# Optimization experiments

Measured on AMD Instinct MI355X. Metric: run time of the kernel, lower is better.

## Reference

```python
import jax, jax.numpy as jnp
import numpy as np

N_NODES = 50000
N_EDGES = 800000
EDGE_F = 96
NODE_F = 256
GLOB_F = 64
HIDDEN = 1024
N_GRAPHS = 8
MLP_IN = NODE_F + 3 * EDGE_F + GLOB_F  # 608


def setup_inputs() -> dict:
    key = jax.random.key(0)
    ks = jax.random.split(key, 9)
    x = jax.random.normal(ks[0], (N_NODES, NODE_F), dtype=jnp.float32)
    edge_attr = jax.random.normal(ks[1], (N_EDGES, EDGE_F), dtype=jnp.float32)
    u = jax.random.normal(ks[2], (N_GRAPHS, GLOB_F), dtype=jnp.float32)
    W1 = jax.random.normal(ks[3], (MLP_IN, HIDDEN), dtype=jnp.float32) * (1.0 / np.sqrt(MLP_IN))
    b1 = jax.random.normal(ks[4], (HIDDEN,), dtype=jnp.float32) * 0.01
    W2 = jax.random.normal(ks[5], (HIDDEN, NODE_F), dtype=jnp.float32) * (1.0 / np.sqrt(HIDDEN))
    b2 = jax.random.normal(ks[6], (NODE_F,), dtype=jnp.float32) * 0.01
    edge_index = jax.random.randint(ks[7], (2, N_EDGES), 0, N_NODES, dtype=jnp.int64 if jax.config.jax_enable_x64 else jnp.int32)
    batch = jnp.sort(jax.random.randint(ks[8], (N_NODES,), 0, N_GRAPHS, dtype=jnp.int32))
    return {"x": x, "edge_attr": edge_attr, "u": u, "W1": W1, "b1": b1,
            "W2": W2, "b2": b2, "edge_index": edge_index, "batch": batch}


def reference(x, edge_attr, u, W1, b1, W2, b2, edge_index, batch):
    col = edge_index[1]  # destination node for each edge
    n = x.shape[0]
    # sum / max / mean segment reductions over edges -> per-node features
    out1 = jax.ops.segment_sum(edge_attr, col, num_segments=n)                     # [N, E_F]
    cnt = jax.ops.segment_sum(jnp.ones((edge_attr.shape[0], 1), edge_attr.dtype), col, num_segments=n)  # [N,1]
    out2 = jax.ops.segment_max(edge_attr, col, num_segments=n)
    out2 = jnp.where(cnt > 0, out2, jnp.zeros_like(out2))  # torch_scatter gives 0 for empty segments
    out3 = out1 / jnp.maximum(cnt, 1.0)                    # mean; 0 for empty segments
    h = jnp.concatenate([x, out1, out2, out3, u[batch]], axis=1)  # [N, 608]
    h = jax.nn.relu(h @ W1 + b1) @ W2 + b2                        # node MLP
    return h + x  # residual
```

## Files before the change

kernel.cpp:

```cpp
#include <hip/hip_runtime.h>
#include <stdint.h>

#define N_NODES 50000
#define N_EDGES 800000
#define EDGE_F  96
#define NODE_F  256
#define GLOB_F  64
#define HIDDEN  1024
#define MLP_IN  608
#define KP      640
#define M_PAD   50176
#define SCAN_BLOCKS 196
#define NT1     10

typedef __bf16 bf16;
typedef __bf16 bf16x8 __attribute__((ext_vector_type(8)));
typedef float  f32x4  __attribute__((ext_vector_type(4)));

typedef __attribute__((address_space(1))) unsigned int gu32;
typedef __attribute__((address_space(3))) unsigned int lu32;

__device__ __forceinline__ void glds16(const void* g, void* l) {
    __builtin_amdgcn_global_load_lds((const gu32*)g, (lu32*)l, 16, 0, 0);
}

static constexpr size_t H_OFF    = 0;
static constexpr size_t H_BYTES  = (size_t)M_PAD * KP * 2;
static constexpr size_t HID_OFF  = H_OFF + H_BYTES;
static constexpr size_t HID_BYTES= (size_t)M_PAD * HIDDEN * 2;
static constexpr size_t W1T_OFF  = HID_OFF + HID_BYTES;
static constexpr size_t W1T_BYTES= (size_t)HIDDEN * KP * 2;
static constexpr size_t W2T_OFF  = W1T_OFF + W1T_BYTES;
static constexpr size_t W2T_BYTES= (size_t)NODE_F * HIDDEN * 2;
static constexpr size_t DEG_OFF  = W2T_OFF + W2T_BYTES;
static constexpr size_t DEG_BYTES= 200192;
static constexpr size_t CUR_OFF  = DEG_OFF + DEG_BYTES;
static constexpr size_t CUR_BYTES= 200192;
static constexpr size_t START_OFF= CUR_OFF + CUR_BYTES;
static constexpr size_t START_BYTES = 200192;
static constexpr size_t EIDS_OFF = START_OFF + START_BYTES;
static constexpr size_t EIDS_BYTES = (size_t)N_EDGES * 4;
static constexpr size_t BSUM_OFF = EIDS_OFF + EIDS_BYTES;
static constexpr size_t BSUM_BYTES = 1024;
static constexpr size_t BOFF_OFF = BSUM_OFF + BSUM_BYTES;

__global__ __launch_bounds__(256) void hist_kernel(const int* __restrict__ col,
                                                   int* __restrict__ deg) {
    int e = blockIdx.x * 256 + threadIdx.x;
    if (e < N_EDGES) atomicAdd(&deg[col[e]], 1);
}

__global__ __launch_bounds__(256) void scan_phase1(const int* __restrict__ deg,
                                                   int* __restrict__ start,
                                                   int* __restrict__ bsum) {
    __shared__ int sc[256];
    const int t = threadIdx.x, b = blockIdx.x;
    const int idx = b * 256 + t;
    int v = (idx < N_NODES) ? deg[idx] : 0;
    sc[t] = v;
    __syncthreads();
    for (int off = 1; off < 256; off <<= 1) {
        int add = (t >= off) ? sc[t - off] : 0;
        __syncthreads();
        sc[t] += add;
        __syncthreads();
    }
    if (idx < N_NODES) start[idx] = sc[t] - v;
    if (t == 255) bsum[b] = sc[255];
}

__global__ __launch_bounds__(256) void scan_phase2(int* __restrict__ bsum,
                                                   int* __restrict__ boff,
                                                   int* __restrict__ start) {
    __shared__ int sc[256];
    const int t = threadIdx.x;
    int v = (t < SCAN_BLOCKS) ? bsum[t] : 0;
    sc[t] = v;
    __syncthreads();
    for (int off = 1; off < 256; off <<= 1) {
        int add = (t >= off) ? sc[t - off] : 0;
        __syncthreads();
        sc[t] += add;
        __syncthreads();
    }
    if (t < SCAN_BLOCKS) boff[t] = sc[t] - v;
    if (t == 255) start[N_NODES] = sc[255];
}

__global__ __launch_bounds__(256) void scan_phase3(int* __restrict__ start,
                                                   const int* __restrict__ boff) {
    const int idx = blockIdx.x * 256 + threadIdx.x;
    if (idx < N_NODES) start[idx] += boff[blockIdx.x];
}

__global__ __launch_bounds__(256) void scatter_kernel(const int* __restrict__ col,
                                                      const int* __restrict__ start,
                                                      int* __restrict__ cursor,
                                                      int* __restrict__ eids) {
    int e = blockIdx.x * 256 + threadIdx.x;
    if (e < N_EDGES) {
        int c = col[e];
        int p = start[c] + atomicAdd(&cursor[c], 1);
        eids[p] = e;
    }
}

#define BH_CHUNK 128
__global__ __launch_bounds__(128) void build_h_kernel(const float* __restrict__ x,
                                                      const float* __restrict__ edge_attr,
                                                      const float* __restrict__ u,
                                                      const int* __restrict__ batch,
                                                      const int* __restrict__ start,
                                                      const int* __restrict__ eids,
                                                      bf16* __restrict__ H) {
    const int n = blockIdx.x;
    const int t = threadIdx.x;
    bf16* row = H + (size_t)n * KP;
    if (n >= N_NODES) {
        for (int c = t; c < KP; c += 128) row[c] = (bf16)0.0f;
        return;
    }
    if (t < 64) {
        float4 v = ((const float4*)(x + (size_t)n * NODE_F))[t];
        row[t * 4 + 0] = (bf16)v.x;
        row[t * 4 + 1] = (bf16)v.y;
        row[t * 4 + 2] = (bf16)v.z;
        row[t * 4 + 3] = (bf16)v.w;
    } else {
        int g = batch[n];
        row[544 + (t - 64)] = (bf16)u[g * GLOB_F + (t - 64)];
    }
    if (t >= 96) row[608 + (t - 96)] = (bf16)0.0f;

    __shared__ int se[BH_CHUNK];
    const int s0 = start[n], s1 = start[n + 1];
    float sm = 0.0f, mx = -3.0e38f;
    for (int base = s0; base < s1; base += BH_CHUNK) {
        const int cnt = min(BH_CHUNK, s1 - base);
        __syncthreads();
        if (t < cnt) se[t] = eids[base + t];
        __syncthreads();
        if (t < EDGE_F) {
            int i = 0;
            for (; i + 8 <= cnt; i += 8) {
                float v0 = edge_attr[(size_t)se[i + 0] * EDGE_F + t];
                float v1 = edge_attr[(size_t)se[i + 1] * EDGE_F + t];
                float v2 = edge_attr[(size_t)se[i + 2] * EDGE_F + t];
                float v3 = edge_attr[(size_t)se[i + 3] * EDGE_F + t];
                float v4 = edge_attr[(size_t)se[i + 4] * EDGE_F + t];
                float v5 = edge_attr[(size_t)se[i + 5] * EDGE_F + t];
                float v6 = edge_attr[(size_t)se[i + 6] * EDGE_F + t];
                float v7 = edge_attr[(size_t)se[i + 7] * EDGE_F + t];
                sm += ((v0 + v1) + (v2 + v3)) + ((v4 + v5) + (v6 + v7));
                float m01 = fmaxf(v0, v1), m23 = fmaxf(v2, v3);
                float m45 = fmaxf(v4, v5), m67 = fmaxf(v6, v7);
                mx = fmaxf(mx, fmaxf(fmaxf(m01, m23), fmaxf(m45, m67)));
            }
            for (; i + 2 <= cnt; i += 2) {
                float v0 = edge_attr[(size_t)se[i + 0] * EDGE_F + t];
                float v1 = edge_attr[(size_t)se[i + 1] * EDGE_F + t];
                sm += v0 + v1;
                mx = fmaxf(mx, fmaxf(v0, v1));
            }
            if (i < cnt) {
                float v = edge_attr[(size_t)se[i] * EDGE_F + t];
                sm += v;
                mx = fmaxf(mx, v);
            }
        }
    }
    if (t < EDGE_F) {
        int d = s1 - s0;
        if (d == 0) mx = 0.0f;
        float mean = sm / fmaxf((float)d, 1.0f);
        row[256 + t] = (bf16)sm;
        row[352 + t] = (bf16)mx;
        row[448 + t] = (bf16)mean;
    }
}

__global__ __launch_bounds__(256) void transpose_kernel(const float* __restrict__ W,
                                                        bf16* __restrict__ Wt,
                                                        int K, int N, int Kpad) {
    __shared__ float tile[32][33];
    const int tx = threadIdx.x & 31, ty = threadIdx.x >> 5;
    const int n0 = blockIdx.x * 32, k0 = blockIdx.y * 32;
    if (k0 < K) {
#pragma unroll
        for (int r = 0; r < 4; r++)
            tile[ty + 8 * r][tx] = W[(size_t)(k0 + ty + 8 * r) * N + (n0 + tx)];
    }
    __syncthreads();
#pragma unroll
    for (int r = 0; r < 4; r++)
        Wt[(size_t)(n0 + ty + 8 * r) * Kpad + (k0 + tx)] =
            (k0 < K) ? (bf16)tile[tx][ty + 8 * r] : (bf16)0.0f;
}

#define VMC(n) asm volatile("s_waitcnt vmcnt(" #n ")" ::: "memory")
#define LGK0   asm volatile("s_waitcnt lgkmcnt(0)" ::: "memory")
#define BARR   __builtin_amdgcn_s_barrier()

__global__ __launch_bounds__(512) void gemm1_kernel(const bf16* __restrict__ H,
                                                    const bf16* __restrict__ Wt,
                                                    const float* __restrict__ b1,
                                                    bf16* __restrict__ hid) {
    __shared__ __align__(16) bf16 As[2][256 * 64];
    __shared__ __align__(16) bf16 Bs[2][256 * 64];
    const int t = threadIdx.x;
    const int wave = t >> 6, lane = t & 63;
    const int quad = lane >> 4, l16 = lane & 15;
    const int wr = wave >> 2;
    const int wc = wave & 3;
    const int bn = blockIdx.x, bm = blockIdx.y;

    f32x4 acc[8][4] = {};
    bf16x8 a[4][2], b[2][2];

    const int srow = t >> 3;
    const int scb  = (((t & 7) ^ (srow & 7)) << 4);
    const char* Ag = (const char*)H  + (size_t)(bm * 256) * (KP * 2);
    const char* Bg = (const char*)Wt + (size_t)(bn * 256) * (KP * 2);
    char* AsB = (char*)&As[0][0];
    char* BsB = (char*)&Bs[0][0];

    const int swzl = (l16 & 7) << 4;
    const int col0 = (quad * 16) ^ swzl;
    const int col1 = (64 + quad * 16) ^ swzl;

#define STG_A(buf, h, kt) do { \
    const char* _s = Ag + (size_t)((h) * 128) * (KP * 2) + (size_t)(kt) * 128; \
    char* _d = AsB + (buf) * 32768 + (h) * 16384 + t * 16; \
    glds16(_s + (size_t)srow * (KP * 2) + scb, _d); \
    glds16(_s + (size_t)(srow + 64) * (KP * 2) + scb, _d + 8192); \
} while (0)
#define STG_B(buf, h, kt) do { \
    const char* _s = Bg + (size_t)((h) * 128) * (KP * 2) + (size_t)(kt) * 128; \
    char* _d = BsB + (buf) * 32768 + (h) * 16384 + t * 16; \
    glds16(_s + (size_t)srow * (KP * 2) + scb, _d); \
    glds16(_s + (size_t)(srow + 64) * (KP * 2) + scb, _d + 8192); \
} while (0)
#define LDA(cbase, mq) do { \
    _Pragma("unroll") for (int i = 0; i < 4; ++i) { \
        const char* _p = (cbase) + (size_t)((mq) * 128 + wr * 64 + i * 16 + l16) * 128; \
        a[i][0] = *(const bf16x8*)(_p + col0); \
        a[i][1] = *(const bf16x8*)(_p + col1); \
    } } while (0)
#define LDB(cbase, nq) do { \
    _Pragma("unroll") for (int j = 0; j < 2; ++j) { \
        const char* _p = (cbase) + (size_t)((nq) * 128 + wc * 32 + j * 16 + l16) * 128; \
        b[j][0] = *(const bf16x8*)(_p + col0); \
        b[j][1] = *(const bf16x8*)(_p + col1); \
    } } while (0)
#define MMAQ(mq, nq) do { \
    __builtin_amdgcn_s_setprio(1); \
    _Pragma("unroll") for (int i = 0; i < 4; ++i) \
    _Pragma("unroll") for (int j = 0; j < 2; ++j) { \
        acc[(mq)*4+i][(nq)*2+j] = __builtin_amdgcn_mfma_f32_16x16x32_bf16(a[i][0], b[j][0], acc[(mq)*4+i][(nq)*2+j], 0, 0, 0); \
        acc[(mq)*4+i][(nq)*2+j] = __builtin_amdgcn_mfma_f32_16x16x32_bf16(a[i][1], b[j][1], acc[(mq)*4+i][(nq)*2+j], 0, 0, 0); \
    } \
    __builtin_amdgcn_s_setprio(0); \
} while (0)

    STG_A(0, 0, 0);
    STG_B(0, 0, 0);
    STG_B(0, 1, 0);
    STG_A(0, 1, 0);
    VMC(4);
    BARR;

#pragma unroll 1
    for (int kt = 0; kt < NT1 - 1; ++kt) {
        const int c = kt & 1, o = c ^ 1;
        const char* Ac = AsB + c * 32768;
        const char* Bc = BsB + c * 32768;
        LDA(Ac, 0); LDB(Bc, 0);
        STG_A(o, 0, kt + 1);
        VMC(4); BARR; LGK0;
        MMAQ(0, 0); BARR;
        LDB(Bc, 1);
        STG_B(o, 0, kt + 1);
        VMC(4); BARR; LGK0;
        MMAQ(0, 1); BARR;
        LDA(Ac, 1);
        STG_B(o, 1, kt + 1);
        BARR; LGK0;
        MMAQ(1, 1); BARR;
        LDB(Bc, 0);
        STG_A(o, 1, kt + 1);
        VMC(4); BARR; LGK0;
        MMAQ(1, 0); BARR;
    }
    {
        const int c = (NT1 - 1) & 1;
        const char* Ac = AsB + c * 32768;
        const char* Bc = BsB + c * 32768;
        LDA(Ac, 0); LDB(Bc, 0); VMC(2); BARR; LGK0; MMAQ(0, 0); BARR;
        LDB(Bc, 1);             VMC(0); BARR; LGK0; MMAQ(0, 1); BARR;
        LDA(Ac, 1);                     BARR; LGK0; MMAQ(1, 1); BARR;
        LDB(Bc, 0);                           LGK0; MMAQ(1, 0);
    }

#pragma unroll
    for (int m = 0; m < 8; ++m) {
        const int mq = m >> 2, i = m & 3;
        const int row0 = bm * 256 + mq * 128 + wr * 64 + i * 16 + quad * 4;
#pragma unroll
        for (int n = 0; n < 4; ++n) {
            const int nq = n >> 1, j = n & 1;
            const int col = bn * 256 + nq * 128 + wc * 32 + j * 16 + l16;
            const float bias = b1[col];
#pragma unroll
            for (int r = 0; r < 4; ++r) {
                float v = acc[m][n][r] + bias;
                v = fmaxf(v, 0.0f);
                hid[(size_t)(row0 + r) * HIDDEN + col] = (bf16)v;
            }
        }
    }
#undef STG_A
#undef STG_B
#undef LDA
#undef LDB
#undef MMAQ
}

__global__ __launch_bounds__(256) void gemm2_kernel(const bf16* __restrict__ Hd,
                                                    const bf16* __restrict__ Wt,
                                                    const float* __restrict__ b2,
                                                    const float* __restrict__ x,
                                                    float* __restrict__ out) {
    __shared__ __align__(16) bf16 As[128 * 32];
    __shared__ __align__(16) bf16 Bs[128 * 32];
    const int t = threadIdx.x;
    const int wave = t >> 6, lane = t & 63;
    const int quad = lane >> 4, l16 = lane & 15;
    const int wm = (wave & 1) << 6, wn = (wave >> 1) << 6;
    const int bm = blockIdx.x, bn = blockIdx.y;

    f32x4 acc[4][4] = {};

    const char* Ag = (const char*)Hd + (size_t)bm * 128 * (HIDDEN * 2);
    const char* Bg = (const char*)Wt + (size_t)bn * 128 * (HIDDEN * 2);
    const int srow = t >> 2, scc = t & 3;
    const size_t rowoff = (size_t)srow * (HIDDEN * 2) + scc * 16;
    char* Al = (char*)As + t * 16;
    char* Bl = (char*)Bs + t * 16;

    for (int k0 = 0; k0 < HIDDEN; k0 += 32) {
        __syncthreads();
        const char* a0 = Ag + rowoff + k0 * 2;
        glds16(a0, Al);
        glds16(a0 + (size_t)64 * (HIDDEN * 2), Al + 4096);
        const char* b0 = Bg + rowoff + k0 * 2;
        glds16(b0, Bl);
        glds16(b0 + (size_t)64 * (HIDDEN * 2), Bl + 4096);
        __syncthreads();
        bf16x8 a[4], b[4];
#pragma unroll
        for (int i = 0; i < 4; i++) a[i] = *(const bf16x8*)&As[(wm + i * 16 + l16) * 32 + quad * 8];
#pragma unroll
        for (int i = 0; i < 4; i++) b[i] = *(const bf16x8*)&Bs[(wn + i * 16 + l16) * 32 + quad * 8];
#pragma unroll
        for (int i = 0; i < 4; i++)
#pragma unroll
            for (int j = 0; j < 4; j++)
                acc[i][j] = __builtin_amdgcn_mfma_f32_16x16x32_bf16(a[i], b[j], acc[i][j], 0, 0, 0);
    }
#pragma unroll
    for (int i = 0; i < 4; i++) {
        int row0 = bm * 128 + wm + i * 16 + quad * 4;
#pragma unroll
        for (int j = 0; j < 4; j++) {
            int col = bn * 128 + wn + j * 16 + l16;
            float bias = b2[col];
#pragma unroll
            for (int r = 0; r < 4; r++) {
                int row = row0 + r;
                if (row < N_NODES) {
                    size_t idx = (size_t)row * NODE_F + col;
                    out[idx] = acc[i][j][r] + bias + x[idx];
                }
            }
        }
    }
}

extern "C" void kernel_launch(void* const* d_in, const int* in_sizes, int n_in,
                              void* d_out, int out_size, void* d_ws, size_t ws_size,
                              hipStream_t stream) {
    const float* x         = (const float*)d_in[0];
    const float* edge_attr = (const float*)d_in[1];
    const float* u         = (const float*)d_in[2];
    const float* W1        = (const float*)d_in[3];
    const float* b1        = (const float*)d_in[4];
    const float* W2        = (const float*)d_in[5];
    const float* b2        = (const float*)d_in[6];
    const int*   edge_index= (const int*)d_in[7];
    const int*   batch     = (const int*)d_in[8];
    float*       out       = (float*)d_out;

    char* ws = (char*)d_ws;
    bf16* H    = (bf16*)(ws + H_OFF);
    bf16* hid  = (bf16*)(ws + HID_OFF);
    bf16* W1t  = (bf16*)(ws + W1T_OFF);
    bf16* W2t  = (bf16*)(ws + W2T_OFF);
    int*  deg  = (int*)(ws + DEG_OFF);
    int*  cur  = (int*)(ws + CUR_OFF);
    int*  start= (int*)(ws + START_OFF);
    int*  eids = (int*)(ws + EIDS_OFF);
    int*  bsum = (int*)(ws + BSUM_OFF);
    int*  boff = (int*)(ws + BOFF_OFF);

    const int* col = edge_index + N_EDGES;

    hipMemsetAsync(ws + DEG_OFF, 0, DEG_BYTES + CUR_BYTES, stream);
    hist_kernel<<<(N_EDGES + 255) / 256, 256, 0, stream>>>(col, deg);
    scan_phase1<<<SCAN_BLOCKS, 256, 0, stream>>>(deg, start, bsum);
    scan_phase2<<<1, 256, 0, stream>>>(bsum, boff, start);
    scan_phase3<<<SCAN_BLOCKS, 256, 0, stream>>>(start, boff);
    scatter_kernel<<<(N_EDGES + 255) / 256, 256, 0, stream>>>(col, start, cur, eids);
    build_h_kernel<<<M_PAD, 128, 0, stream>>>(x, edge_attr, u, batch, start, eids, H);
    transpose_kernel<<<dim3(HIDDEN / 32, KP / 32), 256, 0, stream>>>(W1, W1t, MLP_IN, HIDDEN, KP);
    transpose_kernel<<<dim3(NODE_F / 32, HIDDEN / 32), 256, 0, stream>>>(W2, W2t, HIDDEN, NODE_F, HIDDEN);
    gemm1_kernel<<<dim3(HIDDEN / 256, M_PAD / 256), 512, 0, stream>>>(H, W1t, b1, hid);
    gemm2_kernel<<<dim3(391, 2), 256, 0, stream>>>(hid, W2t, b2, x, out);
}
```

Measured before the change: 769.9 us.

## Rewrite gemm2 as double-buffered 256x256 tile kernel, swizzle gemm1 block order

Replaces the simple single-buffered 128x128 gemm2 with a 512-thread, 256x256-tile kernel that double-buffers LDS via global_load_lds, uses XOR-swizzled LDS layout and overlaps staging of the next k-tile with MFMA work, mirroring the gemm1 structure. Gemm1 launches as a 1D grid with a remapped block index so blocks sharing the same weight column tile are grouped for better L2 reuse. Build_h also packs four bf16 stores into one vector store. The gemm2 grid drops to 196 blocks, fewer than the CU count, which may leave compute units idle.

Measured after the change: 763.6 us. No clear change (-0.8%).

```diff
diff --git a/kernel.cpp b/kernel.cpp
--- a/kernel.cpp
+++ b/kernel.cpp
@@ -12,8 +12,10 @@
 #define M_PAD   50176
 #define SCAN_BLOCKS 196
 #define NT1     10
+#define NT2     16
 
 typedef __bf16 bf16;
+typedef __bf16 bf16x4 __attribute__((ext_vector_type(4)));
 typedef __bf16 bf16x8 __attribute__((ext_vector_type(8)));
 typedef float  f32x4  __attribute__((ext_vector_type(4)));
 
@@ -122,10 +124,9 @@
     }
     if (t < 64) {
         float4 v = ((const float4*)(x + (size_t)n * NODE_F))[t];
-        row[t * 4 + 0] = (bf16)v.x;
-        row[t * 4 + 1] = (bf16)v.y;
-        row[t * 4 + 2] = (bf16)v.z;
-        row[t * 4 + 3] = (bf16)v.w;
+        bf16x4 p;
+        p.x = (bf16)v.x; p.y = (bf16)v.y; p.z = (bf16)v.z; p.w = (bf16)v.w;
+        *(bf16x4*)(row + t * 4) = p;
     } else {
         int g = batch[n];
         row[544 + (t - 64)] = (bf16)u[g * GLOB_F + (t - 64)];
@@ -212,7 +213,9 @@
     const int quad = lane >> 4, l16 = lane & 15;
     const int wr = wave >> 2;
     const int wc = wave & 3;
-    const int bn = blockIdx.x, bm = blockIdx.y;
+    const int orig = blockIdx.x;
+    const int swz  = (orig & 7) * 98 + (orig >> 3);
+    const int bm = swz >> 2, bn = swz & 3;
 
     f32x4 acc[8][4] = {};
     bf16x8 a[4][2], b[2][2];
@@ -325,65 +328,131 @@
 #undef MMAQ
 }
 
-__global__ __launch_bounds__(256) void gemm2_kernel(const bf16* __restrict__ Hd,
+__global__ __launch_bounds__(512) void gemm2_kernel(const bf16* __restrict__ Hd,
                                                     const bf16* __restrict__ Wt,
                                                     const float* __restrict__ b2,
                                                     const float* __restrict__ x,
                                                     float* __restrict__ out) {
-    __shared__ __align__(16) bf16 As[128 * 32];
-    __shared__ __align__(16) bf16 Bs[128 * 32];
+    __shared__ __align__(16) bf16 As[2][256 * 64];
+    __shared__ __align__(16) bf16 Bs[2][256 * 64];
     const int t = threadIdx.x;
     const int wave = t >> 6, lane = t & 63;
     const int quad = lane >> 4, l16 = lane & 15;
-    const int wm = (wave & 1) << 6, wn = (wave >> 1) << 6;
-    const int bm = blockIdx.x, bn = blockIdx.y;
-
-    f32x4 acc[4][4] = {};
-
-    const char* Ag = (const char*)Hd + (size_t)bm * 128 * (HIDDEN * 2);
-    const char* Bg = (const char*)Wt + (size_t)bn * 128 * (HIDDEN * 2);
-    const int srow = t >> 2, scc = t & 3;
-    const size_t rowoff = (size_t)srow * (HIDDEN * 2) + scc * 16;
-    char* Al = (char*)As + t * 16;
-    char* Bl = (char*)Bs + t * 16;
-
-    for (int k0 = 0; k0 < HIDDEN; k0 += 32) {
-        __syncthreads();
-        const char* a0 = Ag + rowoff + k0 * 2;
-        glds16(a0, Al);
-        glds16(a0 + (size_t)64 * (HIDDEN * 2), Al + 4096);
-        const char* b0 = Bg + rowoff + k0 * 2;
-        glds16(b0, Bl);
-        glds16(b0 + (size_t)64 * (HIDDEN * 2), Bl + 4096);
-        __syncthreads();
-        bf16x8 a[4], b[4];
-#pragma unroll
-        for (int i = 0; i < 4; i++) a[i] = *(const bf16x8*)&As[(wm + i * 16 + l16) * 32 + quad * 8];
-#pragma unroll
-        for (int i = 0; i < 4; i++) b[i] = *(const bf16x8*)&Bs[(wn + i * 16 + l16) * 32 + quad * 8];
-#pragma unroll
-        for (int i = 0; i < 4; i++)
-#pragma unroll
-            for (int j = 0; j < 4; j++)
-                acc[i][j] = __builtin_amdgcn_mfma_f32_16x16x32_bf16(a[i], b[j], acc[i][j], 0, 0, 0);
-    }
-#pragma unroll
-    for (int i = 0; i < 4; i++) {
-        int row0 = bm * 128 + wm + i * 16 + quad * 4;
-#pragma unroll
-        for (int j = 0; j < 4; j++) {
-            int col = bn * 128 + wn + j * 16 + l16;
-            float bias = b2[col];
-#pragma unroll
-            for (int r = 0; r < 4; r++) {
-                int row = row0 + r;
+    const int wr = wave >> 2;
+    const int wc = wave & 3;
+    const int bm = blockIdx.x;
+
+    f32x4 acc[8][4] = {};
+    bf16x8 a[4][2], b[2][2];
+
+    const int srow = t >> 3;
+    const int scb  = (((t & 7) ^ (srow & 7)) << 4);
+    const char* Ag = (const char*)Hd + (size_t)(bm * 256) * (HIDDEN * 2);
+    const char* Bg = (const char*)Wt;
+    char* AsB = (char*)&As[0][0];
+    char* BsB = (char*)&Bs[0][0];
+
+    const int swzl = (l16 & 7) << 4;
+    const int col0 = (quad * 16) ^ swzl;
+    const int col1 = (64 + quad * 16) ^ swzl;
+
+#define STG_A2(buf, h, kt) do { \
+    const char* _s = Ag + (size_t)((h) * 128) * (HIDDEN * 2) + (size_t)(kt) * 128; \
+    char* _d = AsB + (buf) * 32768 + (h) * 16384 + t * 16; \
+    glds16(_s + (size_t)srow * (HIDDEN * 2) + scb, _d); \
+    glds16(_s + (size_t)(srow + 64) * (HIDDEN * 2) + scb, _d + 8192); \
+} while (0)
+#define STG_B2(buf, h, kt) do { \
+    const char* _s = Bg + (size_t)((h) * 128) * (HIDDEN * 2) + (size_t)(kt) * 128; \
+    char* _d = BsB + (buf) * 32768 + (h) * 16384 + t * 16; \
+    glds16(_s + (size_t)srow * (HIDDEN * 2) + scb, _d); \
+    glds16(_s + (size_t)(srow + 64) * (HIDDEN * 2) + scb, _d + 8192); \
+} while (0)
+#define LDA2(cbase, mq) do { \
+    _Pragma("unroll") for (int i = 0; i < 4; ++i) { \
+        const char* _p = (cbase) + (size_t)((mq) * 128 + wr * 64 + i * 16 + l16) * 128; \
+        a[i][0] = *(const bf16x8*)(_p + col0); \
+        a[i][1] = *(const bf16x8*)(_p + col1); \
+    } } while (0)
+#define LDB2(cbase, nq) do { \
+    _Pragma("unroll") for (int j = 0; j < 2; ++j) { \
+        const char* _p = (cbase) + (size_t)((nq) * 128 + wc * 32 + j * 16 + l16) * 128; \
+        b[j][0] = *(const bf16x8*)(_p + col0); \
+        b[j][1] = *(const bf16x8*)(_p + col1); \
+    } } while (0)
+#define MMAQ2(mq, nq) do { \
+    __builtin_amdgcn_s_setprio(1); \
+    _Pragma("unroll") for (int i = 0; i < 4; ++i) \
+    _Pragma("unroll") for (int j = 0; j < 2; ++j) { \
+        acc[(mq)*4+i][(nq)*2+j] = __builtin_amdgcn_mfma_f32_16x16x32_bf16(a[i][0], b[j][0], acc[(mq)*4+i][(nq)*2+j], 0, 0, 0); \
+        acc[(mq)*4+i][(nq)*2+j] = __builtin_amdgcn_mfma_f32_16x16x32_bf16(a[i][1], b[j][1], acc[(mq)*4+i][(nq)*2+j], 0, 0, 0); \
+    } \
+    __builtin_amdgcn_s_setprio(0); \
+} while (0)
+
+    STG_A2(0, 0, 0);
+    STG_B2(0, 0, 0);
+    STG_B2(0, 1, 0);
+    STG_A2(0, 1, 0);
+    VMC(4);
+    BARR;
+
+#pragma unroll 1
+    for (int kt = 0; kt < NT2 - 1; ++kt) {
+        const int c = kt & 1, o = c ^ 1;
+        const char* Ac = AsB + c * 32768;
+        const char* Bc = BsB + c * 32768;
+        LDA2(Ac, 0); LDB2(Bc, 0);
+        STG_A2(o, 0, kt + 1);
+        VMC(4); BARR; LGK0;
+        MMAQ2(0, 0); BARR;
+        LDB2(Bc, 1);
+        STG_B2(o, 0, kt + 1);
+        VMC(4); BARR; LGK0;
+        MMAQ2(0, 1); BARR;
+        LDA2(Ac, 1);
+        STG_B2(o, 1, kt + 1);
+        BARR; LGK0;
+        MMAQ2(1, 1); BARR;
+        LDB2(Bc, 0);
+        STG_A2(o, 1, kt + 1);
+        VMC(4); BARR; LGK0;
+        MMAQ2(1, 0); BARR;
+    }
+    {
+        const int c = (NT2 - 1) & 1;
+        const char* Ac = AsB + c * 32768;
+        const char* Bc = BsB + c * 32768;
+        LDA2(Ac, 0); LDB2(Bc, 0); VMC(2); BARR; LGK0; MMAQ2(0, 0); BARR;
+        LDB2(Bc, 1);              VMC(0); BARR; LGK0; MMAQ2(0, 1); BARR;
+        LDA2(Ac, 1);                      BARR; LGK0; MMAQ2(1, 1); BARR;
+        LDB2(Bc, 0);                            LGK0; MMAQ2(1, 0);
+    }
+
+#pragma unroll
+    for (int m = 0; m < 8; ++m) {
+        const int mq = m >> 2, i = m & 3;
+        const int row0 = bm * 256 + mq * 128 + wr * 64 + i * 16 + quad * 4;
+#pragma unroll
+        for (int n = 0; n < 4; ++n) {
+            const int nq = n >> 1, j = n & 1;
+            const int col = nq * 128 + wc * 32 + j * 16 + l16;
+            const float bias = b2[col];
+#pragma unroll
+            for (int r = 0; r < 4; ++r) {
+                const int row = row0 + r;
                 if (row < N_NODES) {
-                    size_t idx = (size_t)row * NODE_F + col;
-                    out[idx] = acc[i][j][r] + bias + x[idx];
+                    const size_t idx = (size_t)row * NODE_F + col;
+                    out[idx] = acc[m][n][r] + bias + x[idx];
                 }
             }
         }
     }
+#undef STG_A2
+#undef STG_B2
+#undef LDA2
+#undef LDB2
+#undef MMAQ2
 }
 
 extern "C" void kernel_launch(void* const* d_in, const int* in_sizes, int n_in,
@@ -423,6 +492,6 @@
     build_h_kernel<<<M_PAD, 128, 0, stream>>>(x, edge_attr, u, batch, start, eids, H);
     transpose_kernel<<<dim3(HIDDEN / 32, KP / 32), 256, 0, stream>>>(W1, W1t, MLP_IN, HIDDEN, KP);
     transpose_kernel<<<dim3(NODE_F / 32, HIDDEN / 32), 256, 0, stream>>>(W2, W2t, HIDDEN, NODE_F, HIDDEN);
-    gemm1_kernel<<<dim3(HIDDEN / 256, M_PAD / 256), 512, 0, stream>>>(H, W1t, b1, hid);
-    gemm2_kernel<<<dim3(391, 2), 256, 0, stream>>>(hid, W2t, b2, x, out);
-}
+    gemm1_kernel<<<dim3(784), 512, 0, stream>>>(H, W1t, b1, hid);
+    gemm2_kernel<<<dim3(196), 512, 0, stream>>>(hid, W2t, b2, x, out);
+}
```
